# Performance work log

Hardware: AMD Instinct MI355X
Metric: run time of the kernel (lower is better)

## Reference

```python
import jax, jax.numpy as jnp
import numpy as np

NUM_GRAPHS = 64
NEG_SLOPE = 0.2


def _gatv2_layer(x, src, dst, edge_attr, Wl, Wr, We, att, b):
    """PyG GATv2Conv (heads=1) with self-loops (fill_value='mean')."""
    n = x.shape[0]
    # self-loop edge_attr = mean of incoming edge_attr per target node
    ones = jnp.ones((src.shape[0],), dtype=x.dtype)
    deg = jax.ops.segment_sum(ones, dst, num_segments=n)
    ea_sum = jax.ops.segment_sum(edge_attr, dst, num_segments=n)
    loop_attr = ea_sum / jnp.maximum(deg, 1.0)[:, None]
    loop = jnp.arange(n)
    src_f = jnp.concatenate([src, loop])
    dst_f = jnp.concatenate([dst, loop])
    ea_f = jnp.concatenate([edge_attr, loop_attr], axis=0)

    xl = x @ Wl              # source transform [N, out]
    xr = x @ Wr              # target transform [N, out]
    ee = ea_f @ We           # edge transform   [E+N, out]

    m = xl[src_f] + xr[dst_f] + ee                      # [E+N, out]
    m = jax.nn.leaky_relu(m, NEG_SLOPE)
    s = m @ att                                         # [E+N] attention logits

    # segment softmax over incoming edges of each target node
    smax = jax.ops.segment_max(s, dst_f, num_segments=n)
    e = jnp.exp(s - smax[dst_f])
    denom = jax.ops.segment_sum(e, dst_f, num_segments=n)
    alpha = e / (denom[dst_f] + 1e-16)

    out = jax.ops.segment_sum(alpha[:, None] * xl[src_f], dst_f, num_segments=n)
    return out + b


def setup_inputs() -> dict:
    key = jax.random.key(0)
    ks = jax.random.split(key, 16)
    N, E, D, ED = 50000, 640000, 128, 16
    sc = 0.1
    inp = {
        "node_features": jax.random.normal(ks[0], (N, D), jnp.float32),
        "edge_index": jax.random.randint(ks[1], (2, E), 0, N, jnp.int64),
        "batch": jnp.sort(jax.random.randint(ks[2], (N,), 0, 64, jnp.int64)),
        "edge_attr": jax.random.normal(ks[3], (E, ED), jnp.float32),
        "Wl1": jax.random.normal(ks[4], (D, D), jnp.float32) * sc,
        "Wr1": jax.random.normal(ks[5], (D, D), jnp.float32) * sc,
        "We1": jax.random.normal(ks[6], (ED, D), jnp.float32) * sc,
        "att1": jax.random.normal(ks[7], (D,), jnp.float32) * sc,
        "b1": jnp.zeros((D,), jnp.float32),
        "Wl2": jax.random.normal(ks[8], (D, D), jnp.float32) * sc,
        "Wr2": jax.random.normal(ks[9], (D, D), jnp.float32) * sc,
        "We2": jax.random.normal(ks[10], (ED, D), jnp.float32) * sc,
        "att2": jax.random.normal(ks[11], (D,), jnp.float32) * sc,
        "b2": jnp.zeros((D,), jnp.float32),
    }
    return inp


def reference(node_features, edge_index, batch, edge_attr,
              Wl1, Wr1, We1, att1, b1, Wl2, Wr2, We2, att2, b2):
    src, dst = edge_index[0], edge_index[1]
    x = _gatv2_layer(node_features, src, dst, edge_attr, Wl1, Wr1, We1, att1, b1)
    x = jax.nn.relu(x)
    x = _gatv2_layer(x, src, dst, edge_attr, Wl2, Wr2, We2, att2, b2)
    x = jax.nn.relu(x)
    # global mean pool over the full node set (node_subset_indices defaults to arange)
    cnt = jax.ops.segment_sum(jnp.ones((x.shape[0],), x.dtype), batch, num_segments=NUM_GRAPHS)
    pooled = jax.ops.segment_sum(x, batch, num_segments=NUM_GRAPHS)
    return pooled / jnp.maximum(cnt, 1.0)[:, None]
```

## Files before the change

### kernel.cpp

```cpp
#include <hip/hip_runtime.h>
#include <hip/hip_bf16.h>
#include <math.h>

#define D 128
#define ED 16
#define NUM_GRAPHS 64
#define SCAN_CHUNK 2048


__global__ void deg_kernel(const int* __restrict__ dst, int* __restrict__ deg, int E) {
  int e = blockIdx.x * 256 + threadIdx.x;
  if (e < E) atomicAdd(&deg[dst[e]], 1);
}

__global__ __launch_bounds__(256) void scan_reduce_kernel(const int* __restrict__ deg,
                                                          int* __restrict__ bsum, int N) {
  int b = blockIdx.x, tid = threadIdx.x;
  int base = b * SCAN_CHUNK + tid * 8;
  int s = 0;
#pragma unroll
  for (int j = 0; j < 8; ++j) {
    int idx = base + j;
    if (idx < N) s += deg[idx];
  }
#pragma unroll
  for (int off = 1; off < 64; off <<= 1) s += __shfl_xor(s, off);
  __shared__ int ws[4];
  int lane = tid & 63, w = tid >> 6;
  if (lane == 0) ws[w] = s;
  __syncthreads();
  if (tid == 0) bsum[b] = ws[0] + ws[1] + ws[2] + ws[3];
}

__global__ void scan_bsum_kernel(const int* __restrict__ bsum, int* __restrict__ boff,
                                 int* __restrict__ rowptrN, int B) {
  int tid = threadIdx.x;
  int v = (tid < B) ? bsum[tid] : 0;
  int x = v;
#pragma unroll
  for (int off = 1; off < 64; off <<= 1) {
    int y = __shfl_up(x, off);
    if (tid >= off) x += y;
  }
  if (tid < B) boff[tid] = x - v;
  if (tid == 63) *rowptrN = x;
}

__global__ __launch_bounds__(256) void scan_write_kernel(const int* __restrict__ deg,
                                                         const int* __restrict__ boff,
                                                         int* __restrict__ rowptr, int N) {
  int b = blockIdx.x, tid = threadIdx.x;
  int lane = tid & 63, w = tid >> 6;
  int base = b * SCAN_CHUNK + tid * 8;
  int v[8];
  int s = 0;
#pragma unroll
  for (int j = 0; j < 8; ++j) {
    int idx = base + j;
    v[j] = (idx < N) ? deg[idx] : 0;
    s += v[j];
  }
  int t = s, x = t;
#pragma unroll
  for (int off = 1; off < 64; off <<= 1) {
    int y = __shfl_up(x, off);
    if (lane >= off) x += y;
  }
  __shared__ int wsum[4];
  if (lane == 63) wsum[w] = x;
  __syncthreads();
  int wexc = 0;
  for (int i = 0; i < w; ++i) wexc += wsum[i];
  int run = boff[b] + wexc + (x - t);
#pragma unroll
  for (int j = 0; j < 8; ++j) {
    int idx = base + j;
    if (idx < N) rowptr[idx] = run;
    run += v[j];
  }
}

__global__ void scatter_kernel(const int* __restrict__ src, const int* __restrict__ dst,
                               const int* __restrict__ rowptr, int* __restrict__ cursor,
                               int2* __restrict__ csr, int E) {
  int e = blockIdx.x * 256 + threadIdx.x;
  if (e >= E) return;
  int d = dst[e];
  int pos = rowptr[d] + atomicAdd(&cursor[d], 1);
  csr[pos] = make_int2(src[e], e);
}

__global__ __launch_bounds__(256) void loopattr_kernel(const float* __restrict__ ea,
                                                       const int* __restrict__ rowptr,
                                                       const int2* __restrict__ csr,
                                                       float* __restrict__ ea_mean, int N) {
  int lane = threadIdx.x & 63;
  int wid = threadIdx.x >> 6;
  int n = blockIdx.x * 4 + wid;
  if (n >= N) return;
  int k = lane & 15, g = lane >> 4;
  int beg = rowptr[n], end = rowptr[n + 1];
  float s = 0.f;
  for (int i = beg + g; i < end; i += 4) {
    int eid = csr[i].y;
    s += ea[(size_t)eid * ED + k];
  }
  s += __shfl_xor(s, 16);
  s += __shfl_xor(s, 32);
  if (g == 0) ea_mean[(size_t)n * ED + k] = s / fmaxf((float)(end - beg), 1.0f);
}


__global__ __launch_bounds__(256) void gemm2_kernel(const float* __restrict__ x,
                                                    const float* __restrict__ Wl,
                                                    const float* __restrict__ Wr,
                                                    float* __restrict__ xl,
                                                    float* __restrict__ xr, int N) {
  __shared__ float xst[D][64];
  __shared__ float ws[16][256];
  int tid = threadIdx.x;
  int base = blockIdx.x * 64;

#pragma unroll
  for (int j = 0; j < 8; ++j) {
    int idx = tid + j * 256;
    int row = idx & 63;
    int c4 = idx >> 6;
    int n = base + row;
    float4 v = make_float4(0.f, 0.f, 0.f, 0.f);
    if (n < N) v = *(const float4*)&x[(size_t)n * D + c4 * 4];
    xst[c4 * 4 + 0][row] = v.x;
    xst[c4 * 4 + 1][row] = v.y;
    xst[c4 * 4 + 2][row] = v.z;
    xst[c4 * 4 + 3][row] = v.w;
  }

  int tn = tid & 15;
  int tc = tid >> 4;
  float acc[4][16];
#pragma unroll
  for (int i = 0; i < 4; ++i)
#pragma unroll
    for (int j = 0; j < 16; ++j) acc[i][j] = 0.f;

  for (int kb = 0; kb < D; kb += 16) {
    __syncthreads();
#pragma unroll
    for (int j = 0; j < 4; ++j) {
      int idx = tid + j * 256;
      int c4 = idx & 63;
      int kk = idx >> 6;
      int c = c4 * 4;
      const float* Wp = (c < D) ? &Wl[(size_t)(kb + kk) * D + c]
                                : &Wr[(size_t)(kb + kk) * D + (c - D)];
      *(float4*)&ws[kk][c] = *(const float4*)Wp;
    }
    __syncthreads();
#pragma unroll
    for (int kk = 0; kk < 16; ++kk) {
      float4 xv = *(float4*)&xst[kb + kk][tn * 4];
      float xa[4] = {xv.x, xv.y, xv.z, xv.w};
      float4 w0 = *(float4*)&ws[kk][tc * 16 + 0];
      float4 w1 = *(float4*)&ws[kk][tc * 16 + 4];
      float4 w2 = *(float4*)&ws[kk][tc * 16 + 8];
      float4 w3 = *(float4*)&ws[kk][tc * 16 + 12];
      float wa[16] = {w0.x, w0.y, w0.z, w0.w, w1.x, w1.y, w1.z, w1.w,
                      w2.x, w2.y, w2.z, w2.w, w3.x, w3.y, w3.z, w3.w};
#pragma unroll
      for (int i = 0; i < 4; ++i)
#pragma unroll
        for (int j = 0; j < 16; ++j) acc[i][j] = fmaf(xa[i], wa[j], acc[i][j]);
    }
  }

#pragma unroll
  for (int i = 0; i < 4; ++i) {
    int n = base + tn * 4 + i;
    if (n >= N) continue;
    float* outp;
    int c;
    if (tc < 8) { outp = xl; c = tc * 16; }
    else        { outp = xr; c = (tc - 8) * 16; }
#pragma unroll
    for (int j4 = 0; j4 < 4; ++j4) {
      float4 v = make_float4(acc[i][j4 * 4 + 0], acc[i][j4 * 4 + 1],
                             acc[i][j4 * 4 + 2], acc[i][j4 * 4 + 3]);
      *(float4*)&outp[(size_t)n * D + c + j4 * 4] = v;
    }
  }
}


__global__ __launch_bounds__(256) void gat_layer_kernel(
    const float* __restrict__ xl, const float* __restrict__ xr,
    const int* __restrict__ rowptr, const int2* __restrict__ csr,
    const float* __restrict__ ea, const float* __restrict__ ea_mean,
    const float* __restrict__ We, const float* __restrict__ att,
    const float* __restrict__ bias, float* __restrict__ y, int N) {
  __shared__ float ea_lds[4][8][ED];
  int lane = threadIdx.x & 63;
  int wid = threadIdx.x >> 6;
  int n = blockIdx.x * 4 + wid;
  if (n >= N) return;

  float weL[ED], weH[ED];
#pragma unroll
  for (int k = 0; k < ED; ++k) {
    float2 w = *(const float2*)&We[k * D + 2 * lane];
    weL[k] = w.x;
    weH[k] = w.y;
  }
  float2 xrv = *(const float2*)&xr[(size_t)n * D + 2 * lane];
  float2 attv = *(const float2*)&att[2 * lane];
  float2 bv = *(const float2*)&bias[2 * lane];

  int beg = rowptr[n], end = rowptr[n + 1];

  float m, denom, acc0, acc1;
  {
    float2 xsl = *(const float2*)&xl[(size_t)n * D + 2 * lane];
    const float4* ap = (const float4*)&ea_mean[(size_t)n * ED];
    float4 q0 = ap[0], q1 = ap[1], q2 = ap[2], q3 = ap[3];
    float av[16] = {q0.x, q0.y, q0.z, q0.w, q1.x, q1.y, q1.z, q1.w,
                    q2.x, q2.y, q2.z, q2.w, q3.x, q3.y, q3.z, q3.w};
    float e0 = 0.f, e1 = 0.f;
#pragma unroll
    for (int k = 0; k < ED; ++k) {
      e0 = fmaf(av[k], weL[k], e0);
      e1 = fmaf(av[k], weH[k], e1);
    }
    float t0 = xsl.x + xrv.x + e0;
    t0 = (t0 > 0.f) ? t0 : 0.2f * t0;
    float t1 = xsl.y + xrv.y + e1;
    t1 = (t1 > 0.f) ? t1 : 0.2f * t1;
    float p = fmaf(t0, attv.x, t1 * attv.y);
#pragma unroll
    for (int off = 32; off > 0; off >>= 1) p += __shfl_xor(p, off);
    m = p;
    denom = 1.f;
    acc0 = xsl.x;
    acc1 = xsl.y;
  }

  int eg = lane >> 4;
  int ek = lane & 15;

  for (int i = beg; i < end; i += 8) {
    int cnt = end - i;
    int idx = i + (lane & 7);
    if (idx >= end) idx = end - 1;
    int2 ce = csr[idx];

    int eid0 = __shfl(ce.y, eg);
    int eid1 = __shfl(ce.y, 4 + eg);
    float a0 = ea[(size_t)eid0 * ED + ek];
    float a1 = ea[(size_t)eid1 * ED + ek];

    float2 xs[8];
#pragma unroll
    for (int j = 0; j < 8; ++j) {
      int sj = __shfl(ce.x, j);
      xs[j] = *(const float2*)&xl[(size_t)sj * D + 2 * lane];
    }

    ea_lds[wid][eg][ek] = a0;
    ea_lds[wid][4 + eg][ek] = a1;

    float pre[8];
#pragma unroll
    for (int j = 0; j < 8; ++j) {
      const float4* eap = (const float4*)&ea_lds[wid][j][0];
      float4 q0 = eap[0], q1 = eap[1], q2 = eap[2], q3 = eap[3];
      float av[16] = {q0.x, q0.y, q0.z, q0.w, q1.x, q1.y, q1.z, q1.w,
                      q2.x, q2.y, q2.z, q2.w, q3.x, q3.y, q3.z, q3.w};
      float e0 = 0.f, e1 = 0.f;
#pragma unroll
      for (int k = 0; k < ED; ++k) {
        e0 = fmaf(av[k], weL[k], e0);
        e1 = fmaf(av[k], weH[k], e1);
      }
      float t0 = xs[j].x + xrv.x + e0;
      t0 = (t0 > 0.f) ? t0 : 0.2f * t0;
      float t1 = xs[j].y + xrv.y + e1;
      t1 = (t1 > 0.f) ? t1 : 0.2f * t1;
      pre[j] = fmaf(t0, attv.x, t1 * attv.y);
    }

#pragma unroll
    for (int off = 32; off > 0; off >>= 1) {
#pragma unroll
      for (int j = 0; j < 8; ++j) pre[j] += __shfl_xor(pre[j], off);
    }

#pragma unroll
    for (int j = 0; j < 8; ++j) {
      if (j < cnt) {
        float p = pre[j];
        if (p > m) {
          float sc = __expf(m - p);
          denom *= sc;
          acc0 *= sc;
          acc1 *= sc;
          m = p;
        }
        float w = __expf(p - m);
        denom += w;
        acc0 = fmaf(w, xs[j].x, acc0);
        acc1 = fmaf(w, xs[j].y, acc1);
      }
    }
  }

  float inv = 1.0f / (denom + 1e-16f);
  float o0 = fmaxf(fmaf(acc0, inv, bv.x), 0.f);
  float o1 = fmaxf(fmaf(acc1, inv, bv.y), 0.f);
  *(float2*)&y[(size_t)n * D + 2 * lane] = make_float2(o0, o1);
}


__global__ __launch_bounds__(128) void pool_kernel(const float* __restrict__ y,
                                                   const int* __restrict__ batch,
                                                   float* __restrict__ out, int N) {
  int g = blockIdx.x;
  int part = blockIdx.y;
  int d = threadIdx.x;
  __shared__ int se[2];
  if (d < 2) {
    int target = g + d;
    int lo = 0, hi = N;
    while (lo < hi) {
      int mid = (lo + hi) >> 1;
      if (batch[mid] < target) lo = mid + 1;
      else hi = mid;
    }
    se[d] = lo;
  }
  __syncthreads();
  int start = se[0], end = se[1];
  int len = end - start;
  int q = (len + 3) >> 2;
  int ps = start + part * q;
  int pe = min(ps + q, end);
  float s0 = 0.f, s1 = 0.f, s2 = 0.f, s3 = 0.f;
  int nn = ps;
  for (; nn + 3 < pe; nn += 4) {
    s0 += y[(size_t)(nn + 0) * D + d];
    s1 += y[(size_t)(nn + 1) * D + d];
    s2 += y[(size_t)(nn + 2) * D + d];
    s3 += y[(size_t)(nn + 3) * D + d];
  }
  for (; nn < pe; ++nn) s0 += y[(size_t)nn * D + d];
  float sum = (s0 + s1) + (s2 + s3);
  float cnt = fmaxf((float)len, 1.0f);
  if (ps < pe) atomicAdd(&out[g * D + d], sum / cnt);
  else if (part == 0 && len <= 0) out[g * D + d] = 0.f;
}


static inline size_t alignup(size_t v) { return (v + 255) & ~(size_t)255; }

extern "C" void kernel_launch(void* const* d_in, const int* in_sizes, int n_in,
                              void* d_out, int out_size, void* d_ws, size_t ws_size,
                              hipStream_t stream) {
  const float* xnode = (const float*)d_in[0];
  const int* eidx = (const int*)d_in[1];
  const int* batch = (const int*)d_in[2];
  const float* eattr = (const float*)d_in[3];
  const float* Wl1 = (const float*)d_in[4];
  const float* Wr1 = (const float*)d_in[5];
  const float* We1 = (const float*)d_in[6];
  const float* att1 = (const float*)d_in[7];
  const float* b1 = (const float*)d_in[8];
  const float* Wl2 = (const float*)d_in[9];
  const float* Wr2 = (const float*)d_in[10];
  const float* We2 = (const float*)d_in[11];
  const float* att2 = (const float*)d_in[12];
  const float* b2 = (const float*)d_in[13];
  float* out = (float*)d_out;

  int N = in_sizes[0] / D;
  int E = in_sizes[3] / ED;
  const int* srcp = eidx;
  const int* dstp = eidx + E;
  int B = (N + SCAN_CHUNK - 1) / SCAN_CHUNK;

  char* p = (char*)d_ws;
  int* rowptr = (int*)p;   p += alignup((size_t)(N + 1) * 4);
  int* deg = (int*)p;      p += alignup((size_t)N * 4);
  int* cursor = (int*)p;   p += alignup((size_t)N * 4);
  int* bsum = (int*)p;     p += alignup((size_t)B * 4);
  int* boff = (int*)p;     p += alignup((size_t)B * 4);
  int2* csr = (int2*)p;    p += alignup((size_t)E * 8);
  float* ea_mean = (float*)p; p += alignup((size_t)N * ED * 4);
  float* xlb = (float*)p;  p += alignup((size_t)N * D * 4);
  float* xrb = (float*)p;  p += alignup((size_t)N * D * 4);
  float* yb = (float*)p;   p += alignup((size_t)N * D * 4);

  hipMemsetAsync(deg, 0, (size_t)N * 4, stream);
  hipMemsetAsync(cursor, 0, (size_t)N * 4, stream);
  hipMemsetAsync(out, 0, (size_t)NUM_GRAPHS * D * 4, stream);

  deg_kernel<<<(E + 255) / 256, 256, 0, stream>>>(dstp, deg, E);
  scan_reduce_kernel<<<B, 256, 0, stream>>>(deg, bsum, N);
  scan_bsum_kernel<<<1, 64, 0, stream>>>(bsum, boff, rowptr + N, B);
  scan_write_kernel<<<B, 256, 0, stream>>>(deg, boff, rowptr, N);
  scatter_kernel<<<(E + 255) / 256, 256, 0, stream>>>(srcp, dstp, rowptr, cursor, csr, E);
  loopattr_kernel<<<(N + 3) / 4, 256, 0, stream>>>(eattr, rowptr, csr, ea_mean, N);

  gemm2_kernel<<<(N + 63) / 64, 256, 0, stream>>>(xnode, Wl1, Wr1, xlb, xrb, N);
  gat_layer_kernel<<<(N + 3) / 4, 256, 0, stream>>>(xlb, xrb, rowptr, csr, eattr, ea_mean,
                                                    We1, att1, b1, yb, N);
  gemm2_kernel<<<(N + 63) / 64, 256, 0, stream>>>(yb, Wl2, Wr2, xlb, xrb, N);
  gat_layer_kernel<<<(N + 3) / 4, 256, 0, stream>>>(xlb, xrb, rowptr, csr, eattr, ea_mean,
                                                    We2, att2, b2, yb, N);
  dim3 pgrid(NUM_GRAPHS, 4);
  pool_kernel<<<pgrid, 128, 0, stream>>>(yb, batch, out, N);
}
```

Before: 727.2 us.

## Process 16 edges per iteration with block-wise online softmax and float4 edge loads

The per-node edge loop now handles 16 edges per iteration instead of 8, loading edge attributes as float4 into a larger LDS tile and using readlane for source indices. The per-edge sequential online-softmax update is replaced with a block-wise max, exp and sum over the 16 edges, followed by a single rescale merge into the running accumulator. This aims to expose more memory-level parallelism for the gathers and to remove the serial dependency chain in the softmax update. It raises register pressure from the 16-wide xs, pre and w arrays, which may lower occupancy, and wastes lanes on nodes with few edges.

```diff
diff --git a/kernel.cpp b/kernel.cpp
--- a/kernel.cpp
+++ b/kernel.cpp
@@ -197,7 +197,7 @@
     const float* __restrict__ ea, const float* __restrict__ ea_mean,
     const float* __restrict__ We, const float* __restrict__ att,
     const float* __restrict__ bias, float* __restrict__ y, int N) {
-  __shared__ float ea_lds[4][8][ED];
+  __shared__ float ea_lds[4][16][16];
   int lane = threadIdx.x & 63;
   int wid = threadIdx.x >> 6;
   int n = blockIdx.x * 4 + wid;
@@ -242,33 +242,27 @@
     acc1 = xsl.y;
   }
 
-  int eg = lane >> 4;
-  int ek = lane & 15;
-
-  for (int i = beg; i < end; i += 8) {
+  const float4* ea4 = (const float4*)ea;
+
+  for (int i = beg; i < end; i += 16) {
     int cnt = end - i;
-    int idx = i + (lane & 7);
+    int idx = i + (lane & 15);
     if (idx >= end) idx = end - 1;
     int2 ce = csr[idx];
 
-    int eid0 = __shfl(ce.y, eg);
-    int eid1 = __shfl(ce.y, 4 + eg);
-    float a0 = ea[(size_t)eid0 * ED + ek];
-    float a1 = ea[(size_t)eid1 * ED + ek];
-
-    float2 xs[8];
-#pragma unroll
-    for (int j = 0; j < 8; ++j) {
-      int sj = __shfl(ce.x, j);
-      xs[j] = *(const float2*)&xl[(size_t)sj * D + 2 * lane];
-    }
-
-    ea_lds[wid][eg][ek] = a0;
-    ea_lds[wid][4 + eg][ek] = a1;
-
-    float pre[8];
-#pragma unroll
-    for (int j = 0; j < 8; ++j) {
+    {
+      int je = lane >> 2;
+      int eid = __shfl(ce.y, je);
+      float4 a = ea4[(size_t)eid * 4 + (lane & 3)];
+      *(float4*)&ea_lds[wid][je][(lane & 3) * 4] = a;
+    }
+
+    float2 xs[16];
+    float pre[16];
+#pragma unroll
+    for (int j = 0; j < 16; ++j) {
+      int srcj = __builtin_amdgcn_readlane(ce.x, j);
+      xs[j] = *(const float2*)&xl[(size_t)srcj * D + 2 * lane];
       const float4* eap = (const float4*)&ea_lds[wid][j][0];
       float4 q0 = eap[0], q1 = eap[1], q2 = eap[2], q3 = eap[3];
       float av[16] = {q0.x, q0.y, q0.z, q0.w, q1.x, q1.y, q1.z, q1.w,
@@ -289,26 +283,44 @@
 #pragma unroll
     for (int off = 32; off > 0; off >>= 1) {
 #pragma unroll
-      for (int j = 0; j < 8; ++j) pre[j] += __shfl_xor(pre[j], off);
-    }
-
-#pragma unroll
-    for (int j = 0; j < 8; ++j) {
-      if (j < cnt) {
-        float p = pre[j];
-        if (p > m) {
-          float sc = __expf(m - p);
-          denom *= sc;
-          acc0 *= sc;
-          acc1 *= sc;
-          m = p;
-        }
-        float w = __expf(p - m);
-        denom += w;
-        acc0 = fmaf(w, xs[j].x, acc0);
-        acc1 = fmaf(w, xs[j].y, acc1);
-      }
-    }
+      for (int j = 0; j < 16; ++j) pre[j] += __shfl_xor(pre[j], off);
+    }
+
+#pragma unroll
+    for (int j = 0; j < 16; ++j)
+      if (j >= cnt) pre[j] = -INFINITY;
+
+    float m0 = fmaxf(pre[0], pre[1]), m1 = fmaxf(pre[2], pre[3]);
+    float m2 = fmaxf(pre[4], pre[5]), m3 = fmaxf(pre[6], pre[7]);
+    float m4 = fmaxf(pre[8], pre[9]), m5 = fmaxf(pre[10], pre[11]);
+    float m6 = fmaxf(pre[12], pre[13]), m7 = fmaxf(pre[14], pre[15]);
+    float ma = fmaxf(fmaxf(m0, m1), fmaxf(m2, m3));
+    float mb = fmaxf(fmaxf(m4, m5), fmaxf(m6, m7));
+    float bm = fmaxf(ma, mb);
+
+    float w[16];
+#pragma unroll
+    for (int j = 0; j < 16; ++j) w[j] = __expf(pre[j] - bm);
+    float d0 = (w[0] + w[1]) + (w[2] + w[3]);
+    float d1 = (w[4] + w[5]) + (w[6] + w[7]);
+    float d2 = (w[8] + w[9]) + (w[10] + w[11]);
+    float d3 = (w[12] + w[13]) + (w[14] + w[15]);
+    float bd = (d0 + d1) + (d2 + d3);
+
+    float ba0 = 0.f, ba1 = 0.f;
+#pragma unroll
+    for (int j = 0; j < 16; ++j) {
+      ba0 = fmaf(w[j], xs[j].x, ba0);
+      ba1 = fmaf(w[j], xs[j].y, ba1);
+    }
+
+    float nm = fmaxf(m, bm);
+    float s1 = __expf(m - nm);
+    float s2 = __expf(bm - nm);
+    denom = denom * s1 + bd * s2;
+    acc0 = acc0 * s1 + ba0 * s2;
+    acc1 = acc1 * s1 + ba1 * s2;
+    m = nm;
   }
 
   float inv = 1.0f / (denom + 1e-16f);
```

Result: slower. 886.1 us (+21.9%).
